# Kernel optimization log

Hardware: AMD Instinct MI355X
Metric: run time of the kernel (lower is better)

Reference implementation:

```python
import jax, jax.numpy as jnp
import numpy as np

SAMPLING_RATIO = 1.0


def gcn_conv(x, src, dst, ew, W, b):
    """PyG GCNConv: h = D^-1/2 (A+I) D^-1/2 (xW) + b, edges weighted by ew.
    Masked edges (ew=0) contribute neither messages nor degree, exactly
    matching running the conv on the subset edge_index."""
    n = x.shape[0]
    h = x @ W                                              # [N, out]
    deg = jax.ops.segment_sum(ew, dst, num_segments=n) + 1.0  # +1 for self-loop
    dinv = jax.lax.rsqrt(deg)                              # deg >= 1, safe
    norm = dinv[src] * dinv[dst] * ew                      # [E]
    agg = jax.ops.segment_sum(h[src] * norm[:, None], dst, num_segments=n)
    return agg + h * (dinv * dinv)[:, None] + b            # self-loop term + bias


def setup_inputs() -> dict:
    key = jax.random.key(0)
    ks = jax.random.split(key, 8)
    N, E, F_IN, HID, OUT = 50000, 800000, 128, 128, 64
    x = jax.random.normal(ks[0], (N, F_IN), dtype=jnp.float32)
    edge_index = jax.random.randint(ks[1], (2, E), 0, N, dtype=jnp.int32)
    edge_rand = jax.random.uniform(ks[2], (E,), dtype=jnp.float32)
    s0 = 1.0 / np.sqrt(F_IN)
    s1 = 1.0 / np.sqrt(HID)
    w0 = jax.random.normal(ks[3], (F_IN, HID), dtype=jnp.float32) * s0
    b0 = jnp.zeros((HID,), dtype=jnp.float32)
    w1 = jax.random.normal(ks[4], (HID, HID), dtype=jnp.float32) * s1
    b1 = jnp.zeros((HID,), dtype=jnp.float32)
    w2 = jax.random.normal(ks[5], (HID, OUT), dtype=jnp.float32) * s1
    b2 = jnp.zeros((OUT,), dtype=jnp.float32)
    return {"x": x, "edge_index": edge_index, "edge_rand": edge_rand,
            "w0": w0, "b0": b0, "w1": w1, "b1": b1, "w2": w2, "b2": b2}


def reference(x, edge_index, edge_rand, w0, b0, w1, b1, w2, b2):
    src, dst = edge_index[0], edge_index[1]
    ones = jnp.ones(src.shape, dtype=x.dtype)
    # first pass over full graph -> tmp_z
    z = jax.nn.relu(gcn_conv(x, src, dst, ones, w0, b0))
    z = jax.nn.relu(gcn_conv(z, src, dst, ones, w1, b1))
    tmp_z = gcn_conv(z, src, dst, ones, w2, b2)
    # edge sampling: gather-dot-sigmoid-threshold (detached mask)
    edge_logit = jnp.sum(tmp_z[src] * tmp_z[dst], axis=-1)
    edge_weight = jax.nn.sigmoid(edge_logit)
    mask = jax.lax.stop_gradient(
        (edge_weight > SAMPLING_RATIO * edge_rand).astype(x.dtype))
    # second pass: sampled edges for hidden layers, full edges for last layer
    h = jax.nn.relu(gcn_conv(x, src, dst, mask, w0, b0))
    h = jax.nn.relu(gcn_conv(h, src, dst, mask, w1, b1))
    out = gcn_conv(h, src, dst, ones, w2, b2)
    return out
```

## Files before the change

kernel.cpp:

```cpp
#include <hip/hip_runtime.h>


typedef __attribute__((ext_vector_type(8))) short bf16x8;
typedef __attribute__((ext_vector_type(4))) float f32x4;

__device__ inline unsigned bfpair(float lo, float hi) {
    unsigned a = __float_as_uint(lo), b = __float_as_uint(hi);
    a = (a + 0x7FFFu + ((a >> 16) & 1u)) >> 16;
    b = (b + 0x7FFFu + ((b >> 16) & 1u)) & 0xFFFF0000u;
    return a | b;
}
__device__ inline unsigned short bf1(float v) {
    unsigned u = __float_as_uint(v);
    return (unsigned short)((u + 0x7FFFu + ((u >> 16) & 1u)) >> 16);
}
__device__ inline void unpack2(unsigned u, float& f0, float& f1) {
    f0 = __uint_as_float(u << 16);
    f1 = __uint_as_float(u & 0xFFFF0000u);
}

__global__ void k_hist(const int* __restrict__ dst, int* __restrict__ indeg, int E) {
    int e = blockIdx.x * blockDim.x + threadIdx.x;
    if (e < E) atomicAdd(&indeg[dst[e]], 1);
}

__global__ void k_scan1(const int* __restrict__ in, int* __restrict__ out,
                        int* __restrict__ bsums, int N) {
    __shared__ int tmp[256];
    int i = blockIdx.x * 256 + threadIdx.x;
    int v = (i < N) ? in[i] : 0;
    tmp[threadIdx.x] = v;
    __syncthreads();
    for (int off = 1; off < 256; off <<= 1) {
        int t = (threadIdx.x >= off) ? tmp[threadIdx.x - off] : 0;
        __syncthreads();
        tmp[threadIdx.x] += t;
        __syncthreads();
    }
    if (i < N) out[i] = tmp[threadIdx.x] - v;
    if (threadIdx.x == 255) bsums[blockIdx.x] = tmp[255];
}

__global__ void k_scan2(int* __restrict__ bsums, int nb) {
    __shared__ int tmp[256];
    int v = (threadIdx.x < nb) ? bsums[threadIdx.x] : 0;
    tmp[threadIdx.x] = v;
    __syncthreads();
    for (int off = 1; off < 256; off <<= 1) {
        int t = (threadIdx.x >= off) ? tmp[threadIdx.x - off] : 0;
        __syncthreads();
        tmp[threadIdx.x] += t;
        __syncthreads();
    }
    if (threadIdx.x < nb) bsums[threadIdx.x] = tmp[threadIdx.x] - v;
}

__global__ void k_scan3(int* __restrict__ out, const int* __restrict__ bsums, int N, int E) {
    int i = blockIdx.x * 256 + threadIdx.x;
    if (i < N) out[i] += bsums[blockIdx.x];
    if (i == 0) out[N] = E;
}

__global__ void k_fill(const int* __restrict__ src, const int* __restrict__ dst,
                       const float* __restrict__ er,
                       const int* __restrict__ csr_off, int* __restrict__ cursor,
                       int2* __restrict__ csr_se, int E) {
    int e = blockIdx.x * blockDim.x + threadIdx.x;
    if (e < E) {
        int d = dst[e];
        int pos = csr_off[d] + atomicAdd(&cursor[d], 1);
        csr_se[pos] = make_int2(src[e], (int)__float_as_uint(er[e]));
    }
}

__global__ void k_dinv(const int* __restrict__ deg, float* __restrict__ dinv, int N) {
    int i = blockIdx.x * blockDim.x + threadIdx.x;
    if (i < N) dinv[i] = 1.0f / sqrtf((float)deg[i] + 1.0f);
}

__global__ void k_coef_full(const int2* __restrict__ csr_se, const float* __restrict__ dinv,
                            float* __restrict__ coef, int E) {
    int i = blockIdx.x * blockDim.x + threadIdx.x;
    if (i < E) coef[i] = dinv[csr_se[i].x];
}

__global__ void k_coef_mask(const int2* __restrict__ csr_se, const float* __restrict__ dinv,
                            const float* __restrict__ survive, float* __restrict__ coef, int E) {
    int i = blockIdx.x * blockDim.x + threadIdx.x;
    if (i < E) coef[i] = dinv[csr_se[i].x] * survive[i];
}

__global__ __launch_bounds__(128) void k_surv(const float* __restrict__ tz,
                                              const int* __restrict__ csr_off,
                                              const int2* __restrict__ csr_se,
                                              float* __restrict__ survive,
                                              int* __restrict__ degm, int N) {
    const int v = blockIdx.x;
    const int l = threadIdx.x & 15;
    const int s = threadIdx.x >> 4;
    const int e0 = csr_off[v];
    const int e1 = csr_off[v + 1];
    const float4 tv = *(const float4*)&tz[(size_t)v * 64 + l * 4];
    int cnt = 0;
    for (int i = e0 + s; i < e1; i += 8) {
        int2 se = csr_se[i];
        const float4 a = *(const float4*)&tz[(size_t)se.x * 64 + l * 4];
        float p = a.x * tv.x + a.y * tv.y + a.z * tv.z + a.w * tv.w;
        p += __shfl_xor(p, 1, 16);
        p += __shfl_xor(p, 2, 16);
        p += __shfl_xor(p, 4, 16);
        p += __shfl_xor(p, 8, 16);
        float sg = 1.0f / (1.0f + expf(-p));
        float m = (sg > __uint_as_float((unsigned)se.y)) ? 1.0f : 0.0f;
        if (l == 0) {
            survive[i] = m;
            cnt += (m != 0.0f) ? 1 : 0;
        }
    }
    __shared__ int sc[8];
    if (l == 0) sc[s] = cnt;
    __syncthreads();
    if (threadIdx.x == 0) {
        int t = 0;
#pragma unroll
        for (int k = 0; k < 8; k++) t += sc[k];
        degm[v] = t;
    }
}

__global__ void k_packw(const float* __restrict__ W, unsigned short* __restrict__ Wpk,
                        int OUTC, int total) {
    int idx = blockIdx.x * 256 + threadIdx.x;
    if (idx >= total) return;
    int l = idx & 63;
    int tk = idx >> 6;
    int kb = tk & 3;
    int ct = tk >> 2;
    unsigned u[4];
#pragma unroll
    for (int i2 = 0; i2 < 4; i2++) {
        float v0 = W[(kb * 32 + ((l >> 4) * 8) + 2 * i2 + 0) * OUTC + ct * 16 + (l & 15)];
        float v1 = W[(kb * 32 + ((l >> 4) * 8) + 2 * i2 + 1) * OUTC + ct * 16 + (l & 15)];
        u[i2] = bfpair(v0, v1);
    }
    *(uint4*)&Wpk[(size_t)idx * 8] = make_uint4(u[0], u[1], u[2], u[3]);
}

__global__ void k_packw3(const float* __restrict__ W, unsigned short* __restrict__ Wp,
                         int OUTC, int total) {
    int idx = blockIdx.x * 256 + threadIdx.x;
    if (idx >= total) return;
    int l = idx & 63;
    int tk = idx >> 6;
    int kb = tk & 3;
    int ct = tk >> 2;
    size_t PL = (size_t)(OUTC / 16) * 4 * 64 * 8;
    unsigned short v0[8], v1[8], v2[8];
#pragma unroll
    for (int i = 0; i < 8; i++) {
        float wv = W[(kb * 32 + ((l >> 4) * 8) + i) * OUTC + ct * 16 + (l & 15)];
        unsigned short h0 = bf1(wv);
        float f0 = __uint_as_float((unsigned)h0 << 16);
        float r1 = wv - f0;
        unsigned short h1 = bf1(r1);
        float f1 = __uint_as_float((unsigned)h1 << 16);
        unsigned short h2 = bf1(r1 - f1);
        v0[i] = h0; v1[i] = h1; v2[i] = h2;
    }
    auto st = [](unsigned short* dst, unsigned short* v) {
        uint4 u;
        u.x = v[0] | ((unsigned)v[1] << 16);
        u.y = v[2] | ((unsigned)v[3] << 16);
        u.z = v[4] | ((unsigned)v[5] << 16);
        u.w = v[6] | ((unsigned)v[7] << 16);
        *(uint4*)dst = u;
    };
    st(&Wp[(size_t)idx * 8], v0);
    st(&Wp[PL + (size_t)idx * 8], v1);
    st(&Wp[2 * PL + (size_t)idx * 8], v2);
}

template <int OUTC, bool WB16>
__global__ __launch_bounds__(256) void k_gemm_split(const float* __restrict__ A,
                                                    const unsigned short* __restrict__ Wp,
                                                    float* __restrict__ Cout,
                                                    unsigned short* __restrict__ Cb, int N) {
    constexpr int CT = OUTC / 16;
    constexpr int PL = CT * 4 * 64 * 8;
    constexpr int LDW = OUTC + 4;
    __shared__ float eps[64 * LDW];
    const int w = threadIdx.x >> 6;
    const int l = threadIdx.x & 63;
    int row = blockIdx.x * 64 + w * 16 + (l & 15);
    int rowc = (row < N) ? row : (N - 1);

    bf16x8 a0[4], a1[4], a2[4];
#pragma unroll
    for (int kb = 0; kb < 4; kb++) {
        const float* pa = &A[(size_t)rowc * 128 + kb * 32 + ((l >> 4) * 8)];
        float4 x0 = *(const float4*)pa;
        float4 x1 = *(const float4*)(pa + 4);
        float xa[8] = {x0.x, x0.y, x0.z, x0.w, x1.x, x1.y, x1.z, x1.w};
#pragma unroll
        for (int i = 0; i < 8; i++) {
            unsigned short h0 = bf1(xa[i]);
            float f0 = __uint_as_float((unsigned)h0 << 16);
            float r1 = xa[i] - f0;
            unsigned short h1 = bf1(r1);
            float f1 = __uint_as_float((unsigned)h1 << 16);
            unsigned short h2 = bf1(r1 - f1);
            a0[kb][i] = (short)h0;
            a1[kb][i] = (short)h1;
            a2[kb][i] = (short)h2;
        }
    }
#pragma unroll
    for (int ct = 0; ct < CT; ct++) {
        f32x4 accA = {0.f, 0.f, 0.f, 0.f};
        f32x4 accB = {0.f, 0.f, 0.f, 0.f};
#pragma unroll
        for (int kb = 0; kb < 4; kb++) {
            const size_t bo = ((size_t)(ct * 4 + kb) * 64 + l) * 8;
            bf16x8 b0 = *(const bf16x8*)&Wp[bo];
            bf16x8 b1 = *(const bf16x8*)&Wp[PL + bo];
            bf16x8 b2 = *(const bf16x8*)&Wp[2 * PL + bo];
            accA = __builtin_amdgcn_mfma_f32_16x16x32_bf16(a0[kb], b0, accA, 0, 0, 0);
            accB = __builtin_amdgcn_mfma_f32_16x16x32_bf16(a0[kb], b1, accB, 0, 0, 0);
            accA = __builtin_amdgcn_mfma_f32_16x16x32_bf16(a1[kb], b0, accA, 0, 0, 0);
            accB = __builtin_amdgcn_mfma_f32_16x16x32_bf16(a0[kb], b2, accB, 0, 0, 0);
            accA = __builtin_amdgcn_mfma_f32_16x16x32_bf16(a1[kb], b1, accA, 0, 0, 0);
            accB = __builtin_amdgcn_mfma_f32_16x16x32_bf16(a2[kb], b0, accB, 0, 0, 0);
            accA = __builtin_amdgcn_mfma_f32_16x16x32_bf16(a1[kb], b2, accA, 0, 0, 0);
            accB = __builtin_amdgcn_mfma_f32_16x16x32_bf16(a2[kb], b1, accB, 0, 0, 0);
        }
#pragma unroll
        for (int r = 0; r < 4; r++) {
            int rr = w * 16 + (l >> 4) * 4 + r;
            eps[rr * LDW + ct * 16 + (l & 15)] = accA[r] + accB[r];
        }
    }
    __syncthreads();
    constexpr int NF4 = 64 * OUTC / 4;
    for (int idx = threadIdx.x; idx < NF4; idx += 256) {
        int rl = idx / (OUTC / 4);
        int cg = idx % (OUTC / 4);
        int grow = blockIdx.x * 64 + rl;
        if (grow < N) {
            const float* sp = &eps[rl * LDW + cg * 4];
            float4 vv = make_float4(sp[0], sp[1], sp[2], sp[3]);
            *(float4*)&Cout[(size_t)grow * OUTC + cg * 4] = vv;
            if (WB16)
                *(uint2*)&Cb[(size_t)grow * OUTC + cg * 4] =
                    make_uint2(bfpair(vv.x, vv.y), bfpair(vv.z, vv.w));
        }
    }
}

template <int OUTC>
__global__ __launch_bounds__(256) void k_gemm_mfma(const unsigned short* __restrict__ A,
                                                   const unsigned short* __restrict__ Wpk,
                                                   unsigned short* __restrict__ C, int N) {
    constexpr int CT = OUTC / 16;
    __shared__ unsigned short eps[64 * OUTC];
    const int w = threadIdx.x >> 6;
    const int l = threadIdx.x & 63;
    const int rowl = (w * 16) + (l & 15);
    int row = blockIdx.x * 64 + rowl;
    int rowc = (row < N) ? row : (N - 1);

    bf16x8 a[4];
#pragma unroll
    for (int kb = 0; kb < 4; kb++)
        a[kb] = *(const bf16x8*)&A[(size_t)rowc * 128 + kb * 32 + ((l >> 4) * 8)];

#pragma unroll
    for (int ct = 0; ct < CT; ct++) {
        f32x4 acc = {0.f, 0.f, 0.f, 0.f};
#pragma unroll
        for (int kb = 0; kb < 4; kb++) {
            bf16x8 b = *(const bf16x8*)&Wpk[((size_t)(ct * 4 + kb) * 64 + l) * 8];
            acc = __builtin_amdgcn_mfma_f32_16x16x32_bf16(a[kb], b, acc, 0, 0, 0);
        }
#pragma unroll
        for (int r = 0; r < 4; r++) {
            int rr = w * 16 + (l >> 4) * 4 + r;
            eps[rr * OUTC + ct * 16 + (l & 15)] = bf1(acc[r]);
        }
    }
    __syncthreads();
    constexpr int NU4 = 64 * OUTC / 8;
    for (int idx = threadIdx.x; idx < NU4; idx += 256) {
        int rl = idx / (OUTC / 8);
        int cg = idx % (OUTC / 8);
        int grow = blockIdx.x * 64 + rl;
        if (grow < N)
            *(uint4*)&C[(size_t)grow * OUTC + cg * 8] = *(const uint4*)&eps[rl * OUTC + cg * 8];
    }
}

template <bool RELU>
__global__ __launch_bounds__(128) void k_agg128(const float* __restrict__ h,
                                                const int* __restrict__ csr_off,
                                                const int2* __restrict__ csr_se,
                                                const float* __restrict__ coef,
                                                const float* __restrict__ dinv,
                                                const float* __restrict__ bias,
                                                float* __restrict__ out, int N) {
    const int v = blockIdx.x;
    const int l = threadIdx.x & 31;
    const int s = threadIdx.x >> 5;
    const int e0 = csr_off[v];
    const int e1 = csr_off[v + 1];
    float4 acc = make_float4(0.f, 0.f, 0.f, 0.f);
    int i = e0 + s;
    for (; i + 4 < e1; i += 8) {
        int sa = csr_se[i].x;      float wa = coef[i];
        int sb = csr_se[i + 4].x;  float wb = coef[i + 4];
        float4 a = *(const float4*)&h[(size_t)sa * 128 + l * 4];
        float4 b = *(const float4*)&h[(size_t)sb * 128 + l * 4];
        acc.x = fmaf(a.x, wa, acc.x); acc.y = fmaf(a.y, wa, acc.y);
        acc.z = fmaf(a.z, wa, acc.z); acc.w = fmaf(a.w, wa, acc.w);
        acc.x = fmaf(b.x, wb, acc.x); acc.y = fmaf(b.y, wb, acc.y);
        acc.z = fmaf(b.z, wb, acc.z); acc.w = fmaf(b.w, wb, acc.w);
    }
    if (i < e1) {
        int sa = csr_se[i].x;
        float wa = coef[i];
        float4 a = *(const float4*)&h[(size_t)sa * 128 + l * 4];
        acc.x = fmaf(a.x, wa, acc.x); acc.y = fmaf(a.y, wa, acc.y);
        acc.z = fmaf(a.z, wa, acc.z); acc.w = fmaf(a.w, wa, acc.w);
    }
    __shared__ float4 red[4][32];
    red[s][l] = acc;
    __syncthreads();
    if (threadIdx.x < 32) {
        float4 r0 = red[0][l], r1 = red[1][l], r2 = red[2][l], r3 = red[3][l];
        float dv = dinv[v];
        float4 hv = *(const float4*)&h[(size_t)v * 128 + l * 4];
        float4 bb = *(const float4*)&bias[l * 4];
        float4 o;
        o.x = dv * ((r0.x + r1.x + r2.x + r3.x) + hv.x * dv) + bb.x;
        o.y = dv * ((r0.y + r1.y + r2.y + r3.y) + hv.y * dv) + bb.y;
        o.z = dv * ((r0.z + r1.z + r2.z + r3.z) + hv.z * dv) + bb.z;
        o.w = dv * ((r0.w + r1.w + r2.w + r3.w) + hv.w * dv) + bb.w;
        if (RELU) {
            o.x = fmaxf(o.x, 0.f); o.y = fmaxf(o.y, 0.f);
            o.z = fmaxf(o.z, 0.f); o.w = fmaxf(o.w, 0.f);
        }
        *(float4*)&out[(size_t)v * 128 + l * 4] = o;
    }
}

__global__ __launch_bounds__(128) void k_agg64(const float* __restrict__ h,
                                               const int* __restrict__ csr_off,
                                               const int2* __restrict__ csr_se,
                                               const float* __restrict__ coef,
                                               const float* __restrict__ dinv,
                                               const float* __restrict__ bias,
                                               float* __restrict__ out, int N) {
    const int v = blockIdx.x;
    const int l = threadIdx.x & 15;
    const int s = threadIdx.x >> 4;
    const int e0 = csr_off[v];
    const int e1 = csr_off[v + 1];
    float4 acc = make_float4(0.f, 0.f, 0.f, 0.f);
    int i = e0 + s;
    for (; i + 8 < e1; i += 16) {
        int sa = csr_se[i].x;      float wa = coef[i];
        int sb = csr_se[i + 8].x;  float wb = coef[i + 8];
        float4 a = *(const float4*)&h[(size_t)sa * 64 + l * 4];
        float4 b = *(const float4*)&h[(size_t)sb * 64 + l * 4];
        acc.x = fmaf(a.x, wa, acc.x); acc.y = fmaf(a.y, wa, acc.y);
        acc.z = fmaf(a.z, wa, acc.z); acc.w = fmaf(a.w, wa, acc.w);
        acc.x = fmaf(b.x, wb, acc.x); acc.y = fmaf(b.y, wb, acc.y);
        acc.z = fmaf(b.z, wb, acc.z); acc.w = fmaf(b.w, wb, acc.w);
    }
    if (i < e1) {
        int sa = csr_se[i].x;
        float wa = coef[i];
        float4 a = *(const float4*)&h[(size_t)sa * 64 + l * 4];
        acc.x = fmaf(a.x, wa, acc.x); acc.y = fmaf(a.y, wa, acc.y);
        acc.z = fmaf(a.z, wa, acc.z); acc.w = fmaf(a.w, wa, acc.w);
    }
    __shared__ float4 red[8][16];
    red[s][l] = acc;
    __syncthreads();
    if (threadIdx.x < 16) {
        float4 aa = make_float4(0.f, 0.f, 0.f, 0.f);
#pragma unroll
        for (int k = 0; k < 8; ++k) {
            float4 r = red[k][l];
            aa.x += r.x; aa.y += r.y; aa.z += r.z; aa.w += r.w;
        }
        float dv = dinv[v];
        float4 hv = *(const float4*)&h[(size_t)v * 64 + l * 4];
        float4 bb = *(const float4*)&bias[l * 4];
        float4 o;
        o.x = dv * (aa.x + hv.x * dv) + bb.x;
        o.y = dv * (aa.y + hv.y * dv) + bb.y;
        o.z = dv * (aa.z + hv.z * dv) + bb.z;
        o.w = dv * (aa.w + hv.w * dv) + bb.w;
        *(float4*)&out[(size_t)v * 64 + l * 4] = o;
    }
}

template <bool RELU>
__global__ __launch_bounds__(128) void k_agg128b(const unsigned short* __restrict__ h,
                                                 const int* __restrict__ csr_off,
                                                 const int2* __restrict__ csr_se,
                                                 const float* __restrict__ coef,
                                                 const float* __restrict__ dinv,
                                                 const float* __restrict__ bias,
                                                 unsigned short* __restrict__ out, int N) {
    const int v = blockIdx.x;
    const int l = threadIdx.x & 15;
    const int s = threadIdx.x >> 4;
    const int e0 = csr_off[v];
    const int e1 = csr_off[v + 1];
    float acc[8];
#pragma unroll
    for (int j = 0; j < 8; j++) acc[j] = 0.f;
    int i = e0 + s;
    for (; i + 8 < e1; i += 16) {
        int sa = csr_se[i].x;      float wa = coef[i];
        int sb = csr_se[i + 8].x;  float wb = coef[i + 8];
        uint4 ua = *(const uint4*)&h[(size_t)sa * 128 + l * 8];
        uint4 ub = *(const uint4*)&h[(size_t)sb * 128 + l * 8];
        float f0, f1;
        unpack2(ua.x, f0, f1); acc[0] = fmaf(f0, wa, acc[0]); acc[1] = fmaf(f1, wa, acc[1]);
        unpack2(ua.y, f0, f1); acc[2] = fmaf(f0, wa, acc[2]); acc[3] = fmaf(f1, wa, acc[3]);
        unpack2(ua.z, f0, f1); acc[4] = fmaf(f0, wa, acc[4]); acc[5] = fmaf(f1, wa, acc[5]);
        unpack2(ua.w, f0, f1); acc[6] = fmaf(f0, wa, acc[6]); acc[7] = fmaf(f1, wa, acc[7]);
        unpack2(ub.x, f0, f1); acc[0] = fmaf(f0, wb, acc[0]); acc[1] = fmaf(f1, wb, acc[1]);
        unpack2(ub.y, f0, f1); acc[2] = fmaf(f0, wb, acc[2]); acc[3] = fmaf(f1, wb, acc[3]);
        unpack2(ub.z, f0, f1); acc[4] = fmaf(f0, wb, acc[4]); acc[5] = fmaf(f1, wb, acc[5]);
        unpack2(ub.w, f0, f1); acc[6] = fmaf(f0, wb, acc[6]); acc[7] = fmaf(f1, wb, acc[7]);
    }
    if (i < e1) {
        int sa = csr_se[i].x;
        float wa = coef[i];
        uint4 ua = *(const uint4*)&h[(size_t)sa * 128 + l * 8];
        float f0, f1;
        unpack2(ua.x, f0, f1); acc[0] = fmaf(f0, wa, acc[0]); acc[1] = fmaf(f1, wa, acc[1]);
        unpack2(ua.y, f0, f1); acc[2] = fmaf(f0, wa, acc[2]); acc[3] = fmaf(f1, wa, acc[3]);
        unpack2(ua.z, f0, f1); acc[4] = fmaf(f0, wa, acc[4]); acc[5] = fmaf(f1, wa, acc[5]);
        unpack2(ua.w, f0, f1); acc[6] = fmaf(f0, wa, acc[6]); acc[7] = fmaf(f1, wa, acc[7]);
    }
    __shared__ float red[8][16][8];
#pragma unroll
    for (int j = 0; j < 8; j += 4)
        *(float4*)&red[s][l][j] = make_float4(acc[j], acc[j + 1], acc[j + 2], acc[j + 3]);
    __syncthreads();
    if (threadIdx.x < 16) {
        int ll = threadIdx.x;
        float rr[8];
#pragma unroll
        for (int j = 0; j < 8; j++) rr[j] = 0.f;
#pragma unroll
        for (int k = 0; k < 8; ++k)
#pragma unroll
            for (int j = 0; j < 8; j++) rr[j] += red[k][ll][j];
        float dv = dinv[v];
        uint4 uh = *(const uint4*)&h[(size_t)v * 128 + ll * 8];
        float hv[8];
        unpack2(uh.x, hv[0], hv[1]); unpack2(uh.y, hv[2], hv[3]);
        unpack2(uh.z, hv[4], hv[5]); unpack2(uh.w, hv[6], hv[7]);
        unsigned u[4];
#pragma unroll
        for (int j2 = 0; j2 < 4; j2++) {
            float o0 = dv * (rr[2 * j2 + 0] + hv[2 * j2 + 0] * dv) + bias[ll * 8 + 2 * j2 + 0];
            float o1 = dv * (rr[2 * j2 + 1] + hv[2 * j2 + 1] * dv) + bias[ll * 8 + 2 * j2 + 1];
            if (RELU) { o0 = fmaxf(o0, 0.f); o1 = fmaxf(o1, 0.f); }
            u[j2] = bfpair(o0, o1);
        }
        *(uint4*)&out[(size_t)v * 128 + ll * 8] = make_uint4(u[0], u[1], u[2], u[3]);
    }
}

__global__ __launch_bounds__(128) void k_agg64b(const unsigned short* __restrict__ h,
                                                const int* __restrict__ csr_off,
                                                const int2* __restrict__ csr_se,
                                                const float* __restrict__ coef,
                                                const float* __restrict__ dinv,
                                                const float* __restrict__ bias,
                                                float* __restrict__ out, int N) {
    const int v = blockIdx.x;
    const int l = threadIdx.x & 7;
    const int s = threadIdx.x >> 3;
    const int e0 = csr_off[v];
    const int e1 = csr_off[v + 1];
    float acc[8];
#pragma unroll
    for (int j = 0; j < 8; j++) acc[j] = 0.f;
    for (int i = e0 + s; i < e1; i += 16) {
        int sa = csr_se[i].x;
        float wa = coef[i];
        uint4 ua = *(const uint4*)&h[(size_t)sa * 64 + l * 8];
        float f0, f1;
        unpack2(ua.x, f0, f1); acc[0] = fmaf(f0, wa, acc[0]); acc[1] = fmaf(f1, wa, acc[1]);
        unpack2(ua.y, f0, f1); acc[2] = fmaf(f0, wa, acc[2]); acc[3] = fmaf(f1, wa, acc[3]);
        unpack2(ua.z, f0, f1); acc[4] = fmaf(f0, wa, acc[4]); acc[5] = fmaf(f1, wa, acc[5]);
        unpack2(ua.w, f0, f1); acc[6] = fmaf(f0, wa, acc[6]); acc[7] = fmaf(f1, wa, acc[7]);
    }
    __shared__ float red[16][8][8];
#pragma unroll
    for (int j = 0; j < 8; j += 4)
        *(float4*)&red[s][l][j] = make_float4(acc[j], acc[j + 1], acc[j + 2], acc[j + 3]);
    __syncthreads();
    if (threadIdx.x < 8) {
        int ll = threadIdx.x;
        float rr[8];
#pragma unroll
        for (int j = 0; j < 8; j++) rr[j] = 0.f;
#pragma unroll
        for (int k = 0; k < 16; ++k)
#pragma unroll
            for (int j = 0; j < 8; j++) rr[j] += red[k][ll][j];
        float dv = dinv[v];
        uint4 uh = *(const uint4*)&h[(size_t)v * 64 + ll * 8];
        float hv[8];
        unpack2(uh.x, hv[0], hv[1]); unpack2(uh.y, hv[2], hv[3]);
        unpack2(uh.z, hv[4], hv[5]); unpack2(uh.w, hv[6], hv[7]);
        float o[8];
#pragma unroll
        for (int j = 0; j < 8; j++) o[j] = dv * (rr[j] + hv[j] * dv) + bias[ll * 8 + j];
        *(float4*)&out[(size_t)v * 64 + ll * 8 + 0] = make_float4(o[0], o[1], o[2], o[3]);
        *(float4*)&out[(size_t)v * 64 + ll * 8 + 4] = make_float4(o[4], o[5], o[6], o[7]);
    }
}

extern "C" void kernel_launch(void* const* d_in, const int* in_sizes, int n_in,
                              void* d_out, int out_size, void* d_ws, size_t ws_size,
                              hipStream_t stream) {
    const float* x  = (const float*)d_in[0];
    const int*   ei = (const int*)d_in[1];
    const float* er = (const float*)d_in[2];
    const float* w0 = (const float*)d_in[3];
    const float* b0 = (const float*)d_in[4];
    const float* w1 = (const float*)d_in[5];
    const float* b1 = (const float*)d_in[6];
    const float* w2 = (const float*)d_in[7];
    const float* b2 = (const float*)d_in[8];
    const int N = in_sizes[0] / 128;
    const int E = in_sizes[2];
    const int* src  = ei;
    const int* dstv = ei + E;
    float* out = (float*)d_out;

    char* p = (char*)d_ws;
    auto alloc = [&](size_t bytes) {
        char* r = p;
        p += (bytes + 255) & ~(size_t)255;
        return r;
    };
    int* indeg     = (int*)alloc((size_t)N * 4);
    int* cursor    = (int*)alloc((size_t)N * 4);
    int* degm      = (int*)alloc((size_t)N * 4);
    int* csr_off   = (int*)alloc((size_t)(N + 1) * 4);
    int* bsums     = (int*)alloc(1024);
    int2* csr_se   = (int2*)alloc((size_t)E * 8);
    float* coefF   = (float*)alloc((size_t)E * 4);
    float* coefM   = (float*)alloc((size_t)E * 4);
    float* survive = (float*)alloc((size_t)E * 4);
    float* dinvF   = (float*)alloc((size_t)N * 4);
    float* dinvM   = (float*)alloc((size_t)N * 4);
    float* hx      = (float*)alloc((size_t)N * 128 * 4);
    unsigned short* hxb = (unsigned short*)alloc((size_t)N * 128 * 2);
    float* wk1     = (float*)alloc((size_t)N * 128 * 4);
    float* wk2     = (float*)alloc((size_t)N * 128 * 4);
    float* tz      = (float*)alloc((size_t)N * 64 * 4);
    unsigned short* w0p3 = (unsigned short*)alloc((size_t)3 * 128 * 128 * 2);
    unsigned short* w1p3 = (unsigned short*)alloc((size_t)3 * 128 * 128 * 2);
    unsigned short* w2p3 = (unsigned short*)alloc((size_t)3 * 128 * 64 * 2);
    unsigned short* w1pk = (unsigned short*)alloc((size_t)128 * 128 * 2);
    unsigned short* w2pk = (unsigned short*)alloc((size_t)128 * 64 * 2);
    unsigned short* wk1b = (unsigned short*)wk1;
    unsigned short* wk2b = (unsigned short*)wk2;

    hipMemsetAsync(indeg, 0, (size_t)N * 4, stream);
    hipMemsetAsync(cursor, 0, (size_t)N * 4, stream);

    const int TB = 256;
    const int ebk = (E + TB - 1) / TB;
    const int nbk = (N + TB - 1) / TB;
    const int nb = (N + 255) / 256;

    k_packw3<<<8, 256, 0, stream>>>(w0, w0p3, 128, 2048);
    k_packw3<<<8, 256, 0, stream>>>(w1, w1p3, 128, 2048);
    k_packw3<<<4, 256, 0, stream>>>(w2, w2p3, 64, 1024);
    k_packw<<<8, 256, 0, stream>>>(w1, w1pk, 128, 2048);
    k_packw<<<4, 256, 0, stream>>>(w2, w2pk, 64, 1024);

    k_hist<<<ebk, TB, 0, stream>>>(dstv, indeg, E);
    k_scan1<<<nb, 256, 0, stream>>>(indeg, csr_off, bsums, N);
    k_scan2<<<1, 256, 0, stream>>>(bsums, nb);
    k_scan3<<<nb, 256, 0, stream>>>(csr_off, bsums, N, E);
    k_fill<<<ebk, TB, 0, stream>>>(src, dstv, er, csr_off, cursor, csr_se, E);
    k_dinv<<<nbk, TB, 0, stream>>>(indeg, dinvF, N);
    k_coef_full<<<ebk, TB, 0, stream>>>(csr_se, dinvF, coefF, E);

    const int gbm = (N + 63) / 64;

    k_gemm_split<128, true><<<gbm, 256, 0, stream>>>(x, w0p3, hx, hxb, N);

    k_agg128<true><<<N, 128, 0, stream>>>(hx, csr_off, csr_se, coefF, dinvF, b0, wk1, N);
    k_gemm_split<128, false><<<gbm, 256, 0, stream>>>(wk1, w1p3, wk2, nullptr, N);
    k_agg128<true><<<N, 128, 0, stream>>>(wk2, csr_off, csr_se, coefF, dinvF, b1, wk1, N);
    k_gemm_split<64, false><<<gbm, 256, 0, stream>>>(wk1, w2p3, wk2, nullptr, N);
    k_agg64<<<N, 128, 0, stream>>>(wk2, csr_off, csr_se, coefF, dinvF, b2, tz, N);

    k_surv<<<N, 128, 0, stream>>>(tz, csr_off, csr_se, survive, degm, N);
    k_dinv<<<nbk, TB, 0, stream>>>(degm, dinvM, N);
    k_coef_mask<<<ebk, TB, 0, stream>>>(csr_se, dinvM, survive, coefM, E);

    k_agg128b<true><<<N, 128, 0, stream>>>(hxb, csr_off, csr_se, coefM, dinvM, b0, wk1b, N);
    k_gemm_mfma<128><<<gbm, 256, 0, stream>>>(wk1b, w1pk, wk2b, N);
    k_agg128b<true><<<N, 128, 0, stream>>>(wk2b, csr_off, csr_se, coefM, dinvM, b1, wk1b, N);
    k_gemm_mfma<64><<<gbm, 256, 0, stream>>>(wk1b, w2pk, wk2b, N);
    k_agg64b<<<N, 128, 0, stream>>>(wk2b, csr_off, csr_se, coefF, dinvF, b2, out, N);
}
```

Measured before the change: 525.1 us.

## Build CSR via two-level bucketed counting sort instead of global atomics

Replaces the global-atomic histogram and fill with a two-pass bucket sort. Edges are first scattered into 64-node buckets using per-block shared-memory counters, then each bucket computes in-degrees and places its edges with shared atomics, writing the full coefficient in the same pass. This removes the separate coefF kernel, the memsets and the extra packw kernels: the mfma GEMMs now reuse the first plane of the split-packed weights. The cost is a staging buffer and a larger scan. The packing assumes src fits in 16 bits, which holds for N=50000.

```diff
diff --git a/kernel.cpp b/kernel.cpp
--- a/kernel.cpp
+++ b/kernel.cpp
@@ -17,11 +17,6 @@
 __device__ inline void unpack2(unsigned u, float& f0, float& f1) {
     f0 = __uint_as_float(u << 16);
     f1 = __uint_as_float(u & 0xFFFF0000u);
-}
-
-__global__ void k_hist(const int* __restrict__ dst, int* __restrict__ indeg, int E) {
-    int e = blockIdx.x * blockDim.x + threadIdx.x;
-    if (e < E) atomicAdd(&indeg[dst[e]], 1);
 }
 
 __global__ void k_scan1(const int* __restrict__ in, int* __restrict__ out,
@@ -61,27 +56,81 @@
     if (i == 0) out[N] = E;
 }
 
-__global__ void k_fill(const int* __restrict__ src, const int* __restrict__ dst,
-                       const float* __restrict__ er,
-                       const int* __restrict__ csr_off, int* __restrict__ cursor,
-                       int2* __restrict__ csr_se, int E) {
-    int e = blockIdx.x * blockDim.x + threadIdx.x;
-    if (e < E) {
+__global__ __launch_bounds__(256) void k_bcount(const int* __restrict__ dst,
+                                                int* __restrict__ cnt, int E, int chunk) {
+    __shared__ int h[1024];
+    for (int i = threadIdx.x; i < 1024; i += 256) h[i] = 0;
+    __syncthreads();
+    int beg = blockIdx.x * chunk, end = min(E, beg + chunk);
+    for (int e = beg + threadIdx.x; e < end; e += 256)
+        atomicAdd(&h[dst[e] >> 6], 1);
+    __syncthreads();
+    for (int b = threadIdx.x; b < 1024; b += 256)
+        cnt[b * 64 + blockIdx.x] = h[b];
+}
+
+__global__ __launch_bounds__(256) void k_bscatter(const int* __restrict__ src,
+                                                  const int* __restrict__ dst,
+                                                  const float* __restrict__ er,
+                                                  const int* __restrict__ sbase,
+                                                  int2* __restrict__ stg, int E, int chunk) {
+    __shared__ int cur[1024];
+    for (int i = threadIdx.x; i < 1024; i += 256) cur[i] = 0;
+    __syncthreads();
+    int beg = blockIdx.x * chunk, end = min(E, beg + chunk);
+    for (int e = beg + threadIdx.x; e < end; e += 256) {
         int d = dst[e];
-        int pos = csr_off[d] + atomicAdd(&cursor[d], 1);
-        csr_se[pos] = make_int2(src[e], (int)__float_as_uint(er[e]));
+        int b = d >> 6;
+        int loc = atomicAdd(&cur[b], 1);
+        int pos = sbase[b * 64 + blockIdx.x] + loc;
+        stg[pos] = make_int2(src[e] | ((d & 63) << 16), (int)__float_as_uint(er[e]));
+    }
+}
+
+__global__ __launch_bounds__(256) void k_bindeg(const int2* __restrict__ stg,
+                                                const int* __restrict__ sbase,
+                                                int* __restrict__ indeg, int N) {
+    __shared__ int cnt[64];
+    if (threadIdx.x < 64) cnt[threadIdx.x] = 0;
+    __syncthreads();
+    int b = blockIdx.x;
+    int beg = sbase[b * 64], end = sbase[(b + 1) * 64];
+    for (int i = beg + threadIdx.x; i < end; i += 256)
+        atomicAdd(&cnt[(stg[i].x >> 16) & 63], 1);
+    __syncthreads();
+    if (threadIdx.x < 64) {
+        int node = b * 64 + threadIdx.x;
+        if (node < N) indeg[node] = cnt[threadIdx.x];
+    }
+}
+
+__global__ __launch_bounds__(256) void k_bfill(const int2* __restrict__ stg,
+                                               const int* __restrict__ sbase,
+                                               const int* __restrict__ csr_off,
+                                               const float* __restrict__ dinvF,
+                                               int2* __restrict__ csr_se,
+                                               float* __restrict__ coefF, int N) {
+    __shared__ int cur[64];
+    int b = blockIdx.x;
+    if (threadIdx.x < 64) {
+        int node = b * 64 + threadIdx.x;
+        cur[threadIdx.x] = (node < N) ? csr_off[node] : 0;
+    }
+    __syncthreads();
+    int beg = sbase[b * 64], end = sbase[(b + 1) * 64];
+    for (int i = beg + threadIdx.x; i < end; i += 256) {
+        int2 se = stg[i];
+        int s = se.x & 0xFFFF;
+        int j = (se.x >> 16) & 63;
+        int pos = atomicAdd(&cur[j], 1);
+        csr_se[pos] = make_int2(s, se.y);
+        coefF[pos] = dinvF[s];
     }
 }
 
 __global__ void k_dinv(const int* __restrict__ deg, float* __restrict__ dinv, int N) {
     int i = blockIdx.x * blockDim.x + threadIdx.x;
     if (i < N) dinv[i] = 1.0f / sqrtf((float)deg[i] + 1.0f);
-}
-
-__global__ void k_coef_full(const int2* __restrict__ csr_se, const float* __restrict__ dinv,
-                            float* __restrict__ coef, int E) {
-    int i = blockIdx.x * blockDim.x + threadIdx.x;
-    if (i < E) coef[i] = dinv[csr_se[i].x];
 }
 
 __global__ void k_coef_mask(const int2* __restrict__ csr_se, const float* __restrict__ dinv,
@@ -128,24 +177,6 @@
     }
 }
 
-__global__ void k_packw(const float* __restrict__ W, unsigned short* __restrict__ Wpk,
-                        int OUTC, int total) {
-    int idx = blockIdx.x * 256 + threadIdx.x;
-    if (idx >= total) return;
-    int l = idx & 63;
-    int tk = idx >> 6;
-    int kb = tk & 3;
-    int ct = tk >> 2;
-    unsigned u[4];
-#pragma unroll
-    for (int i2 = 0; i2 < 4; i2++) {
-        float v0 = W[(kb * 32 + ((l >> 4) * 8) + 2 * i2 + 0) * OUTC + ct * 16 + (l & 15)];
-        float v1 = W[(kb * 32 + ((l >> 4) * 8) + 2 * i2 + 1) * OUTC + ct * 16 + (l & 15)];
-        u[i2] = bfpair(v0, v1);
-    }
-    *(uint4*)&Wpk[(size_t)idx * 8] = make_uint4(u[0], u[1], u[2], u[3]);
-}
-
 __global__ void k_packw3(const float* __restrict__ W, unsigned short* __restrict__ Wp,
                          int OUTC, int total) {
     int idx = blockIdx.x * 256 + threadIdx.x;
@@ -554,14 +585,14 @@
         return r;
     };
     int* indeg     = (int*)alloc((size_t)N * 4);
-    int* cursor    = (int*)alloc((size_t)N * 4);
     int* degm      = (int*)alloc((size_t)N * 4);
     int* csr_off   = (int*)alloc((size_t)(N + 1) * 4);
     int* bsums     = (int*)alloc(1024);
+    int* bcnt      = (int*)alloc((size_t)65536 * 4);
+    int* sbase     = (int*)alloc((size_t)65537 * 4);
     int2* csr_se   = (int2*)alloc((size_t)E * 8);
+    int2* stg      = (int2*)alloc((size_t)E * 8);
     float* coefF   = (float*)alloc((size_t)E * 4);
-    float* coefM   = (float*)alloc((size_t)E * 4);
-    float* survive = (float*)alloc((size_t)E * 4);
     float* dinvF   = (float*)alloc((size_t)N * 4);
     float* dinvM   = (float*)alloc((size_t)N * 4);
     float* hx      = (float*)alloc((size_t)N * 128 * 4);
@@ -572,32 +603,32 @@
     unsigned short* w0p3 = (unsigned short*)alloc((size_t)3 * 128 * 128 * 2);
     unsigned short* w1p3 = (unsigned short*)alloc((size_t)3 * 128 * 128 * 2);
     unsigned short* w2p3 = (unsigned short*)alloc((size_t)3 * 128 * 64 * 2);
-    unsigned short* w1pk = (unsigned short*)alloc((size_t)128 * 128 * 2);
-    unsigned short* w2pk = (unsigned short*)alloc((size_t)128 * 64 * 2);
     unsigned short* wk1b = (unsigned short*)wk1;
     unsigned short* wk2b = (unsigned short*)wk2;
-
-    hipMemsetAsync(indeg, 0, (size_t)N * 4, stream);
-    hipMemsetAsync(cursor, 0, (size_t)N * 4, stream);
+    float* coefM   = (float*)stg;
+    float* survive = (float*)stg + E;
 
     const int TB = 256;
     const int ebk = (E + TB - 1) / TB;
     const int nbk = (N + TB - 1) / TB;
     const int nb = (N + 255) / 256;
+    const int chunk = (E + 63) / 64;
 
     k_packw3<<<8, 256, 0, stream>>>(w0, w0p3, 128, 2048);
     k_packw3<<<8, 256, 0, stream>>>(w1, w1p3, 128, 2048);
     k_packw3<<<4, 256, 0, stream>>>(w2, w2p3, 64, 1024);
-    k_packw<<<8, 256, 0, stream>>>(w1, w1pk, 128, 2048);
-    k_packw<<<4, 256, 0, stream>>>(w2, w2pk, 64, 1024);
-
-    k_hist<<<ebk, TB, 0, stream>>>(dstv, indeg, E);
+
+    k_bcount<<<64, 256, 0, stream>>>(dstv, bcnt, E, chunk);
+    k_scan1<<<256, 256, 0, stream>>>(bcnt, sbase, bsums, 65536);
+    k_scan2<<<1, 256, 0, stream>>>(bsums, 256);
+    k_scan3<<<256, 256, 0, stream>>>(sbase, bsums, 65536, E);
+    k_bscatter<<<64, 256, 0, stream>>>(src, dstv, er, sbase, stg, E, chunk);
+    k_bindeg<<<1024, 256, 0, stream>>>(stg, sbase, indeg, N);
     k_scan1<<<nb, 256, 0, stream>>>(indeg, csr_off, bsums, N);
     k_scan2<<<1, 256, 0, stream>>>(bsums, nb);
     k_scan3<<<nb, 256, 0, stream>>>(csr_off, bsums, N, E);
-    k_fill<<<ebk, TB, 0, stream>>>(src, dstv, er, csr_off, cursor, csr_se, E);
     k_dinv<<<nbk, TB, 0, stream>>>(indeg, dinvF, N);
-    k_coef_full<<<ebk, TB, 0, stream>>>(csr_se, dinvF, coefF, E);
+    k_bfill<<<1024, 256, 0, stream>>>(stg, sbase, csr_off, dinvF, csr_se, coefF, N);
 
     const int gbm = (N + 63) / 64;
 
@@ -614,8 +645,8 @@
     k_coef_mask<<<ebk, TB, 0, stream>>>(csr_se, dinvM, survive, coefM, E);
 
     k_agg128b<true><<<N, 128, 0, stream>>>(hxb, csr_off, csr_se, coefM, dinvM, b0, wk1b, N);
-    k_gemm_mfma<128><<<gbm, 256, 0, stream>>>(wk1b, w1pk, wk2b, N);
+    k_gemm_mfma<128><<<gbm, 256, 0, stream>>>(wk1b, w1p3, wk2b, N);
     k_agg128b<true><<<N, 128, 0, stream>>>(wk2b, csr_off, csr_se, coefM, dinvM, b1, wk1b, N);
-    k_gemm_mfma<64><<<gbm, 256, 0, stream>>>(wk1b, w2pk, wk2b, N);
+    k_gemm_mfma<64><<<gbm, 256, 0, stream>>>(wk1b, w2p3, wk2b, N);
     k_agg64b<<<N, 128, 0, stream>>>(wk2b, csr_off, csr_se, coefF, dinvF, b2, out, N);
 }
```

After: 508.0 us. 3.3% less time.
